# Optimization experiments

Measured on AMD Instinct MI355X. Metric: run time of the kernel, lower is better.

## Reference

```python
import jax, jax.numpy as jnp
import numpy as np

N_EMBD = 512
Q_N_EMBD = 512
N_HEAD = 8
EPS = 1e-5


def _layernorm(x, w, b):
    mu = jnp.mean(x, axis=-1, keepdims=True)
    var = jnp.mean(jnp.square(x - mu), axis=-1, keepdims=True)
    return (x - mu) * jax.lax.rsqrt(var + EPS) * w + b


def setup_inputs() -> dict:
    key = jax.random.key(0)
    ks = jax.random.split(key, 16)
    B, C, H, W = 8, N_EMBD, 32, 32
    s = 1.0 / np.sqrt(N_EMBD)
    inp = {
        "q": jax.random.normal(ks[0], (B, Q_N_EMBD, H, W), jnp.float32),
        "kv": jax.random.normal(ks[1], (B, C, H, W), jnp.float32),
        "ln_kv_w": jnp.ones((N_EMBD,), jnp.float32),
        "ln_kv_b": jnp.zeros((N_EMBD,), jnp.float32),
        "ln_q_w": jnp.ones((Q_N_EMBD,), jnp.float32),
        "ln_q_b": jnp.zeros((Q_N_EMBD,), jnp.float32),
        "Wk": jax.random.normal(ks[2], (N_EMBD, N_EMBD), jnp.float32) * s,
        "bk": jnp.zeros((N_EMBD,), jnp.float32),
        "Wq": jax.random.normal(ks[3], (Q_N_EMBD, N_EMBD), jnp.float32) * s,
        "bq": jnp.zeros((N_EMBD,), jnp.float32),
        "Wv": jax.random.normal(ks[4], (N_EMBD, N_EMBD), jnp.float32) * s,
        "bv": jnp.zeros((N_EMBD,), jnp.float32),
        "Wp": jax.random.normal(ks[5], (N_EMBD, N_EMBD), jnp.float32) * s,
        "bp": jnp.zeros((N_EMBD,), jnp.float32),
    }
    return inp


def reference(q, kv, ln_kv_w, ln_kv_b, ln_q_w, ln_q_b,
              Wk, bk, Wq, bq, Wv, bv, Wp, bp):
    B, C, H, W = kv.shape
    c_q = q.shape[1]
    T = H * W
    hd = C // N_HEAD  # head dim

    # [B, C, H, W] -> [B, T, C] tokens
    kv_t = kv.reshape(B, C, T).transpose(0, 2, 1)
    q_t = q.reshape(B, c_q, T).transpose(0, 2, 1)

    kv_n = _layernorm(kv_t, ln_kv_w, ln_kv_b)
    q_n = _layernorm(q_t, ln_q_w, ln_q_b)

    # projections, split heads: [B, T, C] -> [B, H, T, hd]
    def heads(x):
        return x.reshape(B, T, N_HEAD, hd).transpose(0, 2, 1, 3)

    k = heads(kv_n @ Wk + bk)
    qh = heads(q_n @ Wq + bq)
    v = heads(kv_n @ Wv + bv)

    att = jnp.einsum('bhqd,bhkd->bhqk', qh, k) * (1.0 / np.sqrt(hd))
    att = jax.nn.softmax(att, axis=-1)
    y = jnp.einsum('bhqk,bhkd->bhqd', att, v)
    y = y.transpose(0, 2, 1, 3).reshape(B, T, C)
    y = y @ Wp + bp

    x = kv_t + y  # residual on (pre-LN) kv tokens
    return x.transpose(0, 2, 1).reshape(B, C, H, W)
```

## Files before the change

### kernel.cpp

```cpp
#include <hip/hip_runtime.h>
#include <stdint.h>

#define DI static __device__ __forceinline__

typedef __attribute__((ext_vector_type(8))) short bh8;
typedef __attribute__((ext_vector_type(4))) float f4;

DI short f2bf(float f) {
  unsigned u = __float_as_uint(f);
  u += 0x7fffu + ((u >> 16) & 1u);
  return (short)(u >> 16);
}

DI unsigned pkbf(float a, float b) {
  unsigned ua = __float_as_uint(a) + 0x8000u;
  unsigned ub = __float_as_uint(b) + 0x8000u;
  return __builtin_amdgcn_perm(ub, ua, 0x07060302u);
}

DI unsigned pk4fp8(float a, float b, float c, float d) {
  unsigned w = 0;
  w = __builtin_amdgcn_cvt_pk_fp8_f32(a, b, w, false);
  w = __builtin_amdgcn_cvt_pk_fp8_f32(c, d, w, true);
  return w;
}

DI void gll16(const void* g, void* l) {
  __builtin_amdgcn_global_load_lds(
      (const __attribute__((address_space(1))) unsigned int*)g,
      (__attribute__((address_space(3))) unsigned int*)l, 16, 0, 0);
}

DI f4 mfma16(bh8 a, bh8 b, f4 c) {
  return __builtin_amdgcn_mfma_f32_16x16x32_bf16(a, b, c, 0, 0, 0);
}

DI f4 mfma8(long a, long b, f4 c) {
  return __builtin_amdgcn_mfma_f32_16x16x32_fp8_fp8(a, b, c, 0, 0, 0);
}

DI bh8 ld8(const short* p) { return *(const bh8*)p; }

__global__ __launch_bounds__(256) void prep_k(
    const float* __restrict__ kv, const float* __restrict__ qi,
    const float* __restrict__ kw, const float* __restrict__ kbv,
    const float* __restrict__ qw, const float* __restrict__ qbv,
    const float* __restrict__ Wk, const float* __restrict__ Wq,
    const float* __restrict__ Wv, const float* __restrict__ Wp,
    short* __restrict__ kvn, short* __restrict__ qn,
    short* __restrict__ Wt)
{
  __shared__ char sm[16 * 516 * 4 + 128];
  int role = blockIdx.y;
  int bx = blockIdx.x;
  int tid = threadIdx.x;

  if (role < 4) {
    if (bx >= 256) return;
    float (*ts)[33] = (float(*)[33])sm;
    const float* w = (role == 0) ? Wk : (role == 1) ? Wq : (role == 2) ? Wv : Wp;
    short* o = Wt + ((size_t)role << 18);
    int c0 = (bx & 15) << 5, r0 = (bx >> 4) << 5;
    int tx = tid & 31, ty = tid >> 5;
#pragma unroll
    for (int k = 0; k < 32; k += 8)
      ts[ty + k][tx] = w[((size_t)(r0 + ty + k) << 9) + c0 + tx];
    __syncthreads();
#pragma unroll
    for (int k = 0; k < 32; k += 8)
      o[((size_t)(c0 + ty + k) << 9) + r0 + tx] = f2bf(ts[tx][ty + k]);
    return;
  }

  float (*xs)[516] = (float(*)[516])sm;
  float* smean = (float*)(sm + 16 * 516 * 4);
  float* srstd = smean + 16;
  int which = role - 4;
  const float* x = which ? qi : kv;
  const float* w = which ? qw : kw;
  const float* bb = which ? qbv : kbv;
  short* o = which ? qn : kvn;
  int b = bx >> 6;
  int t0 = (bx & 63) << 4;
  const float* xb = x + ((size_t)b << 19) + (size_t)t0;
#pragma unroll
  for (int k = 0; k < 8; k++) {
    int idx = (k << 8) + tid;
    int c = idx >> 2, tt = (idx & 3) << 2;
    float4 v = *(const float4*)(xb + ((size_t)c << 10) + tt);
    xs[tt + 0][c] = v.x; xs[tt + 1][c] = v.y;
    xs[tt + 2][c] = v.z; xs[tt + 3][c] = v.w;
  }
  __syncthreads();
  {
    int t = tid >> 4, cp = tid & 15;
    float s = 0.f, s2 = 0.f;
#pragma unroll
    for (int k = 0; k < 8; k++) {
      float4 v = *(const float4*)&xs[t][(cp << 2) + (k << 6)];
      s  += v.x + v.y + v.z + v.w;
      s2 += v.x * v.x + v.y * v.y + v.z * v.z + v.w * v.w;
    }
#pragma unroll
    for (int m = 1; m < 16; m <<= 1) {
      s  += __shfl_xor(s,  m);
      s2 += __shfl_xor(s2, m);
    }
    if (cp == 0) {
      float mean = s * (1.f / 512.f);
      float var  = s2 * (1.f / 512.f) - mean * mean;
      smean[t] = mean;
      srstd[t] = rsqrtf(var + 1e-5f);
    }
  }
  __syncthreads();
#pragma unroll
  for (int k = 0; k < 8; k++) {
    int idx = (k << 8) + tid;
    int t = idx >> 7, c = (idx & 127) << 2;
    float4 v = *(const float4*)&xs[t][c];
    float4 wv = *(const float4*)(w + c);
    float4 bv4 = *(const float4*)(bb + c);
    float mu = smean[t], rs = srstd[t];
    float r0 = (v.x - mu) * rs * wv.x + bv4.x;
    float r1 = (v.y - mu) * rs * wv.y + bv4.y;
    float r2 = (v.z - mu) * rs * wv.z + bv4.z;
    float r3 = (v.w - mu) * rs * wv.w + bv4.w;
    uint2 pk; pk.x = pkbf(r0, r1); pk.y = pkbf(r2, r3);
    *(uint2*)(o + (((size_t)(b << 10) + t0 + t) << 9) + c) = pk;
  }
}

__global__ __launch_bounds__(256, 3) void gemm_qkv_k(
    const short* __restrict__ kvn, const short* __restrict__ qn,
    const short* __restrict__ Wt,
    const float* __restrict__ bk, const float* __restrict__ bq,
    const float* __restrict__ bv,
    unsigned char* __restrict__ kb8, unsigned char* __restrict__ qb8,
    unsigned char* __restrict__ vb8)
{
  __shared__ short As[128 * 64];
  __shared__ short Bs[128 * 64];
  int z = blockIdx.z;
  const short* A; const short* Bt; const float* bias;
  int m0, n0;
  if (z == 0)      { A = Wt;             Bt = kvn;            bias = bk; }
  else if (z == 1) { A = Wt + (1 << 18); Bt = qn;             bias = bq; }
  else             { A = kvn;            Bt = Wt + (2 << 18); bias = bv; }
  if (z == 2) { m0 = blockIdx.x << 7; n0 = blockIdx.y << 7; }
  else        { m0 = blockIdx.y << 7; n0 = blockIdx.x << 7; }
  int tid = threadIdx.x;
  int lane = tid & 63, wid = tid >> 6;
  int r = lane & 15, g = lane >> 4;
  int wrow = (wid >> 1) << 6, wcol = (wid & 1) << 6;
  f4 acc[4][4];
#pragma unroll
  for (int i = 0; i < 4; i++)
#pragma unroll
    for (int j = 0; j < 4; j++) {
      acc[i][j][0] = 0.f; acc[i][j][1] = 0.f;
      acc[i][j][2] = 0.f; acc[i][j][3] = 0.f;
    }
  for (int k0 = 0; k0 < 512; k0 += 64) {
    __syncthreads();
#pragma unroll
    for (int it = 0; it < 4; it++) {
      int n = (it << 8) + tid;
      int row = n >> 3;
      int c = (n & 7) ^ (row & 7);
      gll16(A  + ((size_t)(m0 + row) << 9) + k0 + (c << 3), As + (n << 3));
      gll16(Bt + ((size_t)(n0 + row) << 9) + k0 + (c << 3), Bs + (n << 3));
    }
    __syncthreads();
    bh8 a[2][4], b[2][4];
#pragma unroll
    for (int ks = 0; ks < 2; ks++) {
#pragma unroll
      for (int i = 0; i < 4; i++) {
        int R = wrow + (i << 4) + r;
        a[ks][i] = ld8(As + (R << 6) + ((((ks << 2) + g) ^ (R & 7)) << 3));
      }
#pragma unroll
      for (int j = 0; j < 4; j++) {
        int R = wcol + (j << 4) + r;
        b[ks][j] = ld8(Bs + (R << 6) + ((((ks << 2) + g) ^ (R & 7)) << 3));
      }
    }
#pragma unroll
    for (int ks = 0; ks < 2; ks++)
#pragma unroll
      for (int i = 0; i < 4; i++)
#pragma unroll
        for (int j = 0; j < 4; j++)
          acc[i][j] = mfma16(a[ks][i], b[ks][j], acc[i][j]);
  }
#pragma unroll
  for (int i = 0; i < 4; i++) {
#pragma unroll
    for (int j = 0; j < 4; j++) {
      int mm = m0 + wrow + (i << 4) + (g << 2);
      int nn = n0 + wcol + (j << 4) + r;
      if (z == 0) {
        float4 b4 = *(const float4*)(bias + mm);
        int h = mm >> 6, d0 = mm & 63;
        int bb = nn >> 10, tt = nn & 1023;
        int c = tt & 255;
        int p = ((c & 15) << 4) | (c >> 4);
        size_t base = ((size_t)((bb * 8 + h) * 4 + (tt >> 8)) << 14);
        unsigned w = pk4fp8(acc[i][j][0] + b4.x, acc[i][j][1] + b4.y,
                            acc[i][j][2] + b4.z, acc[i][j][3] + b4.w);
        *(unsigned*)(kb8 + base + (p << 6) +
                     (((d0 >> 3) ^ (p & 7)) << 3) + (d0 & 7)) = w;
      } else if (z == 1) {
        float4 b4 = *(const float4*)(bias + mm);
        int h = mm >> 6, d0 = mm & 63;
        int bb = nn >> 10, tt = nn & 1023;
        unsigned w = pk4fp8(acc[i][j][0] + b4.x, acc[i][j][1] + b4.y,
                            acc[i][j][2] + b4.z, acc[i][j][3] + b4.w);
        *(unsigned*)(qb8 + ((((size_t)(bb * 8 + h)) << 10) + tt) * 64 + d0) = w;
      } else {
        float bvv = bias[nn];
        int h = nn >> 6, d = nn & 63;
        int bb = mm >> 10, tt = mm & 1023;
        int tb = (tt & 255) >> 3;
        size_t base = ((size_t)((bb * 8 + h) * 4 + (tt >> 8)) << 14);
        unsigned w = pk4fp8(acc[i][j][0] + bvv, acc[i][j][1] + bvv,
                            acc[i][j][2] + bvv, acc[i][j][3] + bvv);
        *(unsigned*)(vb8 + base + (d << 8) +
                     ((tb ^ (d & 31)) << 3) + (tt & 7)) = w;
      }
    }
  }
}

__global__ __launch_bounds__(256, 3) void gemm_proj_k(
    const short* __restrict__ A, const short* __restrict__ Bt,
    const float* __restrict__ bias, float* __restrict__ outp,
    const float* __restrict__ resid)
{
  __shared__ short As[64 * 64];
  __shared__ short Bs[128 * 64];
  int m0 = blockIdx.y << 6, n0 = blockIdx.x << 7;
  int tid = threadIdx.x;
  int lane = tid & 63, wid = tid >> 6;
  int r = lane & 15, g = lane >> 4;
  int wrow = (wid >> 1) << 5, wcol = (wid & 1) << 6;
  f4 acc[2][4];
#pragma unroll
  for (int i = 0; i < 2; i++)
#pragma unroll
    for (int j = 0; j < 4; j++) {
      acc[i][j][0] = 0.f; acc[i][j][1] = 0.f;
      acc[i][j][2] = 0.f; acc[i][j][3] = 0.f;
    }
  for (int k0 = 0; k0 < 512; k0 += 64) {
    __syncthreads();
#pragma unroll
    for (int it = 0; it < 2; it++) {
      int n = (it << 8) + tid;
      int row = n >> 3;
      int c = (n & 7) ^ (row & 7);
      gll16(A + ((size_t)(m0 + row) << 9) + k0 + (c << 3), As + (n << 3));
    }
#pragma unroll
    for (int it = 0; it < 4; it++) {
      int n = (it << 8) + tid;
      int row = n >> 3;
      int c = (n & 7) ^ (row & 7);
      gll16(Bt + ((size_t)(n0 + row) << 9) + k0 + (c << 3), Bs + (n << 3));
    }
    __syncthreads();
    bh8 a[2][2], b[2][4];
#pragma unroll
    for (int ks = 0; ks < 2; ks++) {
#pragma unroll
      for (int i = 0; i < 2; i++) {
        int R = wrow + (i << 4) + r;
        a[ks][i] = ld8(As + (R << 6) + ((((ks << 2) + g) ^ (R & 7)) << 3));
      }
#pragma unroll
      for (int j = 0; j < 4; j++) {
        int R = wcol + (j << 4) + r;
        b[ks][j] = ld8(Bs + (R << 6) + ((((ks << 2) + g) ^ (R & 7)) << 3));
      }
    }
#pragma unroll
    for (int ks = 0; ks < 2; ks++)
#pragma unroll
      for (int i = 0; i < 2; i++)
#pragma unroll
        for (int j = 0; j < 4; j++)
          acc[i][j] = mfma16(a[ks][i], b[ks][j], acc[i][j]);
  }
#pragma unroll
  for (int i = 0; i < 2; i++) {
#pragma unroll
    for (int j = 0; j < 4; j++) {
      int mm = m0 + wrow + (i << 4) + (g << 2);
      int nn = n0 + wcol + (j << 4) + r;
      int bb = nn >> 10, t = nn & 1023;
#pragma unroll
      for (int q = 0; q < 4; q++) {
        int m = mm + q;
        size_t ad = ((((size_t)bb << 9) + m) << 10) + t;
        outp[ad] = acc[i][j][q] + bias[m] + resid[ad];
      }
    }
  }
}

__global__ __launch_bounds__(256, 2) void attn_k(
    const unsigned char* __restrict__ qb8, const unsigned char* __restrict__ kb8,
    const unsigned char* __restrict__ vb8, short* __restrict__ yo)
{
  __shared__ char Ks[16384];
  __shared__ char Vs[16384];
  __shared__ char Ps[32768];
  int h = blockIdx.x, b = blockIdx.z;
  int qt0 = blockIdx.y << 7;
  int tid = threadIdx.x, lane = tid & 63, wid = tid >> 6;
  int r = lane & 15, g = lane >> 4;
  int wbase = wid << 5;
  size_t bh = (size_t)(b * 8 + h);
  const unsigned char* Qg = qb8 + ((bh << 10) + qt0) * 64;
  const unsigned char* Kg = kb8 + (bh << 16);
  const unsigned char* Vg = vb8 + (bh << 16);

  long qf8[2][2];
#pragma unroll
  for (int i = 0; i < 2; i++)
#pragma unroll
    for (int ksd = 0; ksd < 2; ksd++)
      qf8[i][ksd] = *(const long*)(Qg +
          ((size_t)(wbase + (i << 4) + r) << 6) + (((ksd << 2) + g) << 3));

  const long ONES = 0x3838383838383838L;

  f4 oac[2][4], sacc[2];
#pragma unroll
  for (int i = 0; i < 2; i++) {
#pragma unroll
    for (int jn = 0; jn < 4; jn++) {
      oac[i][jn][0] = 0.f; oac[i][jn][1] = 0.f;
      oac[i][jn][2] = 0.f; oac[i][jn][3] = 0.f;
    }
    sacc[i][0] = 0.f; sacc[i][1] = 0.f; sacc[i][2] = 0.f; sacc[i][3] = 0.f;
  }

  const float csc = 0.18033688011112042f;

  for (int ck = 0; ck < 4; ck++) {
    __syncthreads();
#pragma unroll
    for (int it = 0; it < 4; it++) {
      int n = ((it << 8) + tid) << 4;
      gll16(Kg + (ck << 14) + n, Ks + n);
      gll16(Vg + (ck << 14) + n, Vs + n);
    }
    __syncthreads();

    long kf[2][16];
    f4 s[16];
#pragma unroll
    for (int i = 0; i < 2; i++) {
#pragma unroll
      for (int j = 0; j < 16; j++) {
        s[j][0] = 0.f; s[j][1] = 0.f; s[j][2] = 0.f; s[j][3] = 0.f;
      }
#pragma unroll
      for (int ksd = 0; ksd < 2; ksd++)
#pragma unroll
        for (int j = 0; j < 16; j++) {
          if (i == 0)
            kf[ksd][j] = *(const long*)(Ks + (((j << 4) + r) << 6) +
                            ((((ksd << 2) + g) ^ (r & 7)) << 3));
          s[j] = mfma8(qf8[i][ksd], kf[ksd][j], s[j]);
        }
#pragma unroll
      for (int q = 0; q < 4; q++) {
        float e[16];
#pragma unroll
        for (int j = 0; j < 16; j++)
          e[j] = __builtin_amdgcn_exp2f(
                     fminf(fmaf(s[j][q], csc, -3.0f), 8.5f));
        int w0 = 0, w1 = 0, w2 = 0, w3 = 0;
        w0 = __builtin_amdgcn_cvt_pk_fp8_f32(e[0],  e[1],  w0, false);
        w0 = __builtin_amdgcn_cvt_pk_fp8_f32(e[2],  e[3],  w0, true);
        w1 = __builtin_amdgcn_cvt_pk_fp8_f32(e[4],  e[5],  w1, false);
        w1 = __builtin_amdgcn_cvt_pk_fp8_f32(e[6],  e[7],  w1, true);
        w2 = __builtin_amdgcn_cvt_pk_fp8_f32(e[8],  e[9],  w2, false);
        w2 = __builtin_amdgcn_cvt_pk_fp8_f32(e[10], e[11], w2, true);
        w3 = __builtin_amdgcn_cvt_pk_fp8_f32(e[12], e[13], w3, false);
        w3 = __builtin_amdgcn_cvt_pk_fp8_f32(e[14], e[15], w3, true);
        long plo = ((long)(unsigned)w0) | ((long)w1 << 32);
        long phi = ((long)(unsigned)w2) | ((long)w3 << 32);
        int row = wbase + (i << 4) + (g << 2) + q;
        int cc = r ^ (row & 15);
        *(long*)(Ps + (row << 8) + (cc << 4))     = plo;
        *(long*)(Ps + (row << 8) + (cc << 4) + 8) = phi;
      }
    }

#pragma unroll
    for (int ks = 0; ks < 8; ks++) {
      long ap[2];
#pragma unroll
      for (int i = 0; i < 2; i++) {
        int row = wbase + (i << 4) + r;
        int cc = ((ks << 1) + (g >> 1)) ^ (row & 15);
        ap[i] = *(const long*)(Ps + (row << 8) + (cc << 4) + ((g & 1) << 3));
        sacc[i] = mfma8(ap[i], ONES, sacc[i]);
      }
#pragma unroll
      for (int jn = 0; jn < 4; jn++) {
        int d = (jn << 4) + r;
        long bv8 = *(const long*)(Vs + (d << 8) +
                      ((((ks << 2) + g) ^ (d & 31)) << 3));
#pragma unroll
        for (int i = 0; i < 2; i++)
          oac[i][jn] = mfma8(ap[i], bv8, oac[i][jn]);
      }
    }
  }

#pragma unroll
  for (int i = 0; i < 2; i++)
#pragma unroll
    for (int q = 0; q < 4; q++) {
      float inv = 1.f / (sacc[i][q] + 1e-20f);
      int trow = qt0 + wbase + (i << 4) + (g << 2) + q;
      size_t base = (((size_t)(b << 10) + trow) << 9) + (h << 6);
#pragma unroll
      for (int jn = 0; jn < 4; jn++)
        yo[base + (jn << 4) + r] = f2bf(oac[i][jn][q] * inv);
    }
}

extern "C" void kernel_launch(void* const* d_in, const int* in_sizes, int n_in,
                              void* d_out, int out_size, void* d_ws, size_t ws_size,
                              hipStream_t stream)
{
  const float* q    = (const float*)d_in[0];
  const float* kv   = (const float*)d_in[1];
  const float* lnkw = (const float*)d_in[2];
  const float* lnkb = (const float*)d_in[3];
  const float* lnqw = (const float*)d_in[4];
  const float* lnqb = (const float*)d_in[5];
  const float* Wk   = (const float*)d_in[6];
  const float* bk   = (const float*)d_in[7];
  const float* Wq   = (const float*)d_in[8];
  const float* bq   = (const float*)d_in[9];
  const float* Wv   = (const float*)d_in[10];
  const float* bv   = (const float*)d_in[11];
  const float* Wp   = (const float*)d_in[12];
  const float* bp   = (const float*)d_in[13];

  char* ws = (char*)d_ws;
  const size_t SZ = (size_t)8192 * 512 * 2;
  short* buf0 = (short*)(ws);
  short* qn   = (short*)(ws + SZ);
  unsigned char* kb8 = (unsigned char*)(ws + 2 * SZ);
  unsigned char* qb8 = (unsigned char*)(ws + 3 * SZ);
  unsigned char* vb8 = (unsigned char*)(ws + 4 * SZ);
  short* Wt   = (short*)(ws + 5 * SZ);
  if (ws_size < 5 * SZ + 4 * 512 * 512 * 2) return;

  prep_k<<<dim3(512, 6), 256, 0, stream>>>(kv, q, lnkw, lnkb, lnqw, lnqb,
                                           Wk, Wq, Wv, Wp, buf0, qn, Wt);
  gemm_qkv_k<<<dim3(64, 4, 3), 256, 0, stream>>>(buf0, qn, Wt, bk, bq, bv,
                                                 kb8, qb8, vb8);
  attn_k<<<dim3(8, 8, 8), 256, 0, stream>>>(qb8, kb8, vb8, buf0);
  gemm_proj_k<<<dim3(64, 8), 256, 0, stream>>>(Wt + (3 << 18), buf0, bp,
                                               (float*)d_out, kv);
}
```

Measured before the change: 164.0 us.

## Keep attention probabilities in registers via transposed S and permuted V layout

The attention kernel now computes S transposed (K as the A operand) so each lane's exp values already sit in the register layout the PV MFMA A-operand expects. This removes the 32KB shared-memory P buffer and its store/load round trip. The V store layout in the QKV GEMM is permuted to match the new key ordering. Row sums are accumulated in scalar registers and reduced with shuffles instead of an extra MFMA against ones. Each block now handles 64 query rows instead of 128, which doubles the grid and raises the occupancy hint to 4, but K/V tiles are reloaded twice as often overall.

```diff
diff --git a/kernel.cpp b/kernel.cpp
--- a/kernel.cpp
+++ b/kernel.cpp
@@ -222,7 +222,8 @@
         float bvv = bias[nn];
         int h = nn >> 6, d = nn & 63;
         int bb = mm >> 10, tt = mm & 1023;
-        int tb = (tt & 255) >> 3;
+        int t8 = tt & 255;
+        int tb = (((t8 >> 4) & 3) << 3) | (((t8 >> 3) & 1) << 2) | (t8 >> 6);
         size_t base = ((size_t)((bb * 8 + h) * 4 + (tt >> 8)) << 14);
         unsigned w = pk4fp8(acc[i][j][0] + bvv, acc[i][j][1] + bvv,
                             acc[i][j][2] + bvv, acc[i][j][3] + bvv);
@@ -309,43 +310,34 @@
   }
 }
 
-__global__ __launch_bounds__(256, 2) void attn_k(
+__global__ __launch_bounds__(256, 4) void attn_k(
     const unsigned char* __restrict__ qb8, const unsigned char* __restrict__ kb8,
     const unsigned char* __restrict__ vb8, short* __restrict__ yo)
 {
   __shared__ char Ks[16384];
   __shared__ char Vs[16384];
-  __shared__ char Ps[32768];
   int h = blockIdx.x, b = blockIdx.z;
-  int qt0 = blockIdx.y << 7;
-  int tid = threadIdx.x, lane = tid & 63, wid = tid >> 6;
+  int qt0 = blockIdx.y << 6;
+  int tid = threadIdx.x, lane = tid & 63;
   int r = lane & 15, g = lane >> 4;
-  int wbase = wid << 5;
+  int wbase = (tid >> 6) << 4;
   size_t bh = (size_t)(b * 8 + h);
   const unsigned char* Qg = qb8 + ((bh << 10) + qt0) * 64;
   const unsigned char* Kg = kb8 + (bh << 16);
   const unsigned char* Vg = vb8 + (bh << 16);
 
-  long qf8[2][2];
-#pragma unroll
-  for (int i = 0; i < 2; i++)
-#pragma unroll
-    for (int ksd = 0; ksd < 2; ksd++)
-      qf8[i][ksd] = *(const long*)(Qg +
-          ((size_t)(wbase + (i << 4) + r) << 6) + (((ksd << 2) + g) << 3));
-
-  const long ONES = 0x3838383838383838L;
-
-  f4 oac[2][4], sacc[2];
-#pragma unroll
-  for (int i = 0; i < 2; i++) {
-#pragma unroll
-    for (int jn = 0; jn < 4; jn++) {
-      oac[i][jn][0] = 0.f; oac[i][jn][1] = 0.f;
-      oac[i][jn][2] = 0.f; oac[i][jn][3] = 0.f;
-    }
-    sacc[i][0] = 0.f; sacc[i][1] = 0.f; sacc[i][2] = 0.f; sacc[i][3] = 0.f;
-  }
+  long qf8[2];
+#pragma unroll
+  for (int ksd = 0; ksd < 2; ksd++)
+    qf8[ksd] = *(const long*)(Qg +
+        ((size_t)(wbase + r) << 6) + (((ksd << 2) + g) << 3));
+
+  f4 oac[4];
+#pragma unroll
+  for (int jn = 0; jn < 4; jn++) {
+    oac[jn][0] = 0.f; oac[jn][1] = 0.f; oac[jn][2] = 0.f; oac[jn][3] = 0.f;
+  }
+  float rs = 0.f;
 
   const float csc = 0.18033688011112042f;
 
@@ -359,81 +351,61 @@
     }
     __syncthreads();
 
-    long kf[2][16];
-    f4 s[16];
-#pragma unroll
-    for (int i = 0; i < 2; i++) {
-#pragma unroll
-      for (int j = 0; j < 16; j++) {
-        s[j][0] = 0.f; s[j][1] = 0.f; s[j][2] = 0.f; s[j][3] = 0.f;
+    unsigned Wq[4][4];
+#pragma unroll
+    for (int jq = 0; jq < 4; jq++) {
+      f4 s[4];
+#pragma unroll
+      for (int jj = 0; jj < 4; jj++) {
+        s[jj][0] = 0.f; s[jj][1] = 0.f; s[jj][2] = 0.f; s[jj][3] = 0.f;
       }
 #pragma unroll
       for (int ksd = 0; ksd < 2; ksd++)
 #pragma unroll
-        for (int j = 0; j < 16; j++) {
-          if (i == 0)
-            kf[ksd][j] = *(const long*)(Ks + (((j << 4) + r) << 6) +
-                            ((((ksd << 2) + g) ^ (r & 7)) << 3));
-          s[j] = mfma8(qf8[i][ksd], kf[ksd][j], s[j]);
+        for (int jj = 0; jj < 4; jj++) {
+          int j = (jq << 2) + jj;
+          long kf = *(const long*)(Ks + (((j << 4) + r) << 6) +
+                        ((((ksd << 2) + g) ^ (r & 7)) << 3));
+          s[jj] = mfma8(kf, qf8[ksd], s[jj]);
         }
 #pragma unroll
-      for (int q = 0; q < 4; q++) {
-        float e[16];
-#pragma unroll
-        for (int j = 0; j < 16; j++)
-          e[j] = __builtin_amdgcn_exp2f(
-                     fminf(fmaf(s[j][q], csc, -3.0f), 8.5f));
-        int w0 = 0, w1 = 0, w2 = 0, w3 = 0;
-        w0 = __builtin_amdgcn_cvt_pk_fp8_f32(e[0],  e[1],  w0, false);
-        w0 = __builtin_amdgcn_cvt_pk_fp8_f32(e[2],  e[3],  w0, true);
-        w1 = __builtin_amdgcn_cvt_pk_fp8_f32(e[4],  e[5],  w1, false);
-        w1 = __builtin_amdgcn_cvt_pk_fp8_f32(e[6],  e[7],  w1, true);
-        w2 = __builtin_amdgcn_cvt_pk_fp8_f32(e[8],  e[9],  w2, false);
-        w2 = __builtin_amdgcn_cvt_pk_fp8_f32(e[10], e[11], w2, true);
-        w3 = __builtin_amdgcn_cvt_pk_fp8_f32(e[12], e[13], w3, false);
-        w3 = __builtin_amdgcn_cvt_pk_fp8_f32(e[14], e[15], w3, true);
-        long plo = ((long)(unsigned)w0) | ((long)w1 << 32);
-        long phi = ((long)(unsigned)w2) | ((long)w3 << 32);
-        int row = wbase + (i << 4) + (g << 2) + q;
-        int cc = r ^ (row & 15);
-        *(long*)(Ps + (row << 8) + (cc << 4))     = plo;
-        *(long*)(Ps + (row << 8) + (cc << 4) + 8) = phi;
+      for (int qq = 0; qq < 4; qq++) {
+        float e0 = __builtin_amdgcn_exp2f(fminf(fmaf(s[0][qq], csc, -3.0f), 8.5f));
+        float e1 = __builtin_amdgcn_exp2f(fminf(fmaf(s[1][qq], csc, -3.0f), 8.5f));
+        float e2 = __builtin_amdgcn_exp2f(fminf(fmaf(s[2][qq], csc, -3.0f), 8.5f));
+        float e3 = __builtin_amdgcn_exp2f(fminf(fmaf(s[3][qq], csc, -3.0f), 8.5f));
+        rs += (e0 + e1) + (e2 + e3);
+        Wq[qq][jq] = pk4fp8(e0, e1, e2, e3);
       }
     }
 
 #pragma unroll
     for (int ks = 0; ks < 8; ks++) {
-      long ap[2];
-#pragma unroll
-      for (int i = 0; i < 2; i++) {
-        int row = wbase + (i << 4) + r;
-        int cc = ((ks << 1) + (g >> 1)) ^ (row & 15);
-        ap[i] = *(const long*)(Ps + (row << 8) + (cc << 4) + ((g & 1) << 3));
-        sacc[i] = mfma8(ap[i], ONES, sacc[i]);
-      }
+      long ap = (long)(unsigned)Wq[ks >> 1][(ks & 1) << 1] |
+                ((long)Wq[ks >> 1][((ks & 1) << 1) + 1] << 32);
 #pragma unroll
       for (int jn = 0; jn < 4; jn++) {
         int d = (jn << 4) + r;
         long bv8 = *(const long*)(Vs + (d << 8) +
                       ((((ks << 2) + g) ^ (d & 31)) << 3));
-#pragma unroll
-        for (int i = 0; i < 2; i++)
-          oac[i][jn] = mfma8(ap[i], bv8, oac[i][jn]);
-      }
-    }
-  }
-
-#pragma unroll
-  for (int i = 0; i < 2; i++)
-#pragma unroll
-    for (int q = 0; q < 4; q++) {
-      float inv = 1.f / (sacc[i][q] + 1e-20f);
-      int trow = qt0 + wbase + (i << 4) + (g << 2) + q;
-      size_t base = (((size_t)(b << 10) + trow) << 9) + (h << 6);
-#pragma unroll
-      for (int jn = 0; jn < 4; jn++)
-        yo[base + (jn << 4) + r] = f2bf(oac[i][jn][q] * inv);
-    }
+        oac[jn] = mfma8(ap, bv8, oac[jn]);
+      }
+    }
+  }
+
+  rs += __shfl_xor(rs, 16);
+  rs += __shfl_xor(rs, 32);
+
+#pragma unroll
+  for (int qq = 0; qq < 4; qq++) {
+    float rsq = __shfl(rs, (g << 2) + qq);
+    float inv = 1.f / (rsq + 1e-20f);
+    int trow = qt0 + wbase + (g << 2) + qq;
+    size_t base = (((size_t)(b << 10) + trow) << 9) + (h << 6);
+#pragma unroll
+    for (int jn = 0; jn < 4; jn++)
+      yo[base + (jn << 4) + r] = f2bf(oac[jn][qq] * inv);
+  }
 }
 
 extern "C" void kernel_launch(void* const* d_in, const int* in_sizes, int n_in,
@@ -469,7 +441,7 @@
                                            Wk, Wq, Wv, Wp, buf0, qn, Wt);
   gemm_qkv_k<<<dim3(64, 4, 3), 256, 0, stream>>>(buf0, qn, Wt, bk, bq, bv,
                                                  kb8, qb8, vb8);
-  attn_k<<<dim3(8, 8, 8), 256, 0, stream>>>(qb8, kb8, vb8, buf0);
+  attn_k<<<dim3(8, 16, 8), 256, 0, stream>>>(qb8, kb8, vb8, buf0);
   gemm_proj_k<<<dim3(64, 8), 256, 0, stream>>>(Wt + (3 << 18), buf0, bp,
                                                (float*)d_out, kv);
 }
```

Result: no change. 165.5 us (+0.9%).
